# Optimization experiments

Hardware: AMD Instinct MI355X
Metric: run time of the kernel (lower is better)

Reference implementation:

```python
import jax, jax.numpy as jnp
import numpy as np

N, E, D, NHID, NOUT, G = 50000, 800000, 128, 512, 768, 512
EPS = 1e-5

def setup_inputs() -> dict:
    key = jax.random.key(0)
    ks = jax.random.split(key, 20)
    rn = lambda k, s: jax.random.normal(k, s, jnp.float32) * 0.05
    inp = {
        'x': jax.random.normal(ks[0], (N, D), jnp.float32),
        'edge_index': jax.random.randint(ks[1], (2, E), 0, N, jnp.int32),
        'batch': jnp.sort(jax.random.randint(ks[2], (N,), 0, G, jnp.int32)),
        # GCN convs 1..3 (weights stored [in, out])
        'W1': rn(ks[3], (D, D)), 'b1': jnp.zeros((D,), jnp.float32),
        'W2': rn(ks[4], (D, D)), 'b2': jnp.zeros((D,), jnp.float32),
        'W3': rn(ks[5], (D, D)), 'b3': jnp.zeros((D,), jnp.float32),
        # GAT attention layer (1 head)
        'Wa': rn(ks[6], (D, D)), 'ba': jnp.zeros((D,), jnp.float32),
        'a_src': rn(ks[7], (D,)), 'a_dst': rn(ks[8], (D,)),
        # BatchNorms: bn1, bn2, bn3, bn_attention stacked [4, D]
        'bn_gamma': jnp.ones((4, D), jnp.float32),
        'bn_beta': jnp.zeros((4, D), jnp.float32),
        # MLP head
        'Wm1': rn(ks[9], (D, NHID)), 'bm1': jnp.zeros((NHID,), jnp.float32),
        'Wm2': rn(ks[10], (NHID, NHID)), 'bm2': jnp.zeros((NHID,), jnp.float32),
        'Wm3': rn(ks[11], (NHID, NHID)), 'bm3': jnp.zeros((NHID,), jnp.float32),
        'Wm4': rn(ks[12], (NHID, NOUT)), 'bm4': jnp.zeros((NOUT,), jnp.float32),
    }
    return inp

def _bn(h, g, b):
    # BatchNorm1d over nodes, training-mode batch stats (biased variance)
    m = jnp.mean(h, axis=0)
    v = jnp.var(h, axis=0)
    return (h - m) * jax.lax.rsqrt(v + EPS) * g + b

def _gcn(x, W, b, src, dst, deg_isqrt):
    h = x @ W                               # [N, D]
    norm = deg_isqrt[src] * deg_isqrt[dst]  # [E+N]
    msg = h[src] * norm[:, None]            # gather + scale
    return jax.ops.segment_sum(msg, dst, num_segments=N) + b

def _gat(x, W, b, a_src, a_dst, src, dst):
    h = x @ W
    e = jax.nn.leaky_relu((h @ a_src)[src] + (h @ a_dst)[dst], 0.2)  # [E+N]
    m = jax.ops.segment_max(e, dst, num_segments=N)
    ex = jnp.exp(e - m[dst])
    den = jax.ops.segment_sum(ex, dst, num_segments=N)
    alpha = ex / den[dst]
    out = jax.ops.segment_sum(alpha[:, None] * h[src], dst, num_segments=N)
    return out + b

def reference(x, edge_index, batch, W1, b1, W2, b2, W3, b3, Wa, ba, a_src, a_dst,
              bn_gamma, bn_beta, Wm1, bm1, Wm2, bm2, Wm3, bm3, Wm4, bm4):
    # add self-loops (PyG GCNConv / GATConv default)
    loops = jnp.arange(N, dtype=edge_index.dtype)
    src = jnp.concatenate([edge_index[0], loops])
    dst = jnp.concatenate([edge_index[1], loops])
    deg = jax.ops.segment_sum(jnp.ones_like(dst, jnp.float32), dst, num_segments=N)
    deg_isqrt = jax.lax.rsqrt(deg)  # deg >= 1 thanks to self-loops

    relu = jax.nn.relu
    x = relu(_bn(_gcn(x, W1, b1, src, dst, deg_isqrt), bn_gamma[0], bn_beta[0])) + x
    x = relu(_bn(_gcn(x, W2, b2, src, dst, deg_isqrt), bn_gamma[1], bn_beta[1])) + x
    x = relu(_bn(_gcn(x, W3, b3, src, dst, deg_isqrt), bn_gamma[2], bn_beta[2])) + x
    x = relu(_bn(_gat(x, Wa, ba, a_src, a_dst, src, dst), bn_gamma[3], bn_beta[3])) + x

    # global mean pool over graphs
    counts = jax.ops.segment_sum(jnp.ones((N,), jnp.float32), batch, num_segments=G)
    pooled = jax.ops.segment_sum(x, batch, num_segments=G) / jnp.maximum(counts, 1.0)[:, None]

    h = relu(pooled @ Wm1 + bm1)
    h = relu(h @ Wm2 + bm2)
    h = relu(h @ Wm3 + bm3)
    return h @ Wm4 + bm4
```

## Files before the change

### kernel.cpp

```cpp
#include <hip/hip_runtime.h>
#include <stdint.h>

#define Nn   50000
#define Ee   800000
#define Dd   128
#define Gg   512
#define NHIDc 512
#define NOUTc 768
#define EPSf 1e-5f
#define CAP  64
#define PRNG 6250

#define OFF_CNT    0ul
#define OFF_ISQ    200192ul
#define OFF_ES     400384ul
#define OFF_ED     600576ul
#define OFF_STATS  800768ul
#define OFF_POOLED 801792ul
#define OFF_M1     1063936ul
#define OFF_M2     2112512ul
#define OFF_COL    3161088ul
#define OFF_H      15961088ul
#define OFF_AGG    28761088ul
#define OFF_XCUR   41561088ul

#define BF_LO(u) __uint_as_float((u) << 16)
#define BF_HI(u) __uint_as_float((u) & 0xffff0000u)

typedef __attribute__((ext_vector_type(8))) short bf16x8;
typedef __attribute__((ext_vector_type(4))) float f32x4;

__device__ inline uint32_t bfpack(float x, float y) {
    uint32_t ux = __float_as_uint(x), uy = __float_as_uint(y);
    ux += 0x7fff + ((ux >> 16) & 1);
    uy += 0x7fff + ((uy >> 16) & 1);
    return (ux >> 16) | (uy & 0xffff0000u);
}
__device__ inline short bf1(float x) {
    uint32_t u = __float_as_uint(x);
    u += 0x7fff + ((u >> 16) & 1);
    return (short)(u >> 16);
}
__device__ inline float wred16(float v) {
    v += __shfl_xor(v, 1); v += __shfl_xor(v, 2);
    v += __shfl_xor(v, 4); v += __shfl_xor(v, 8);
    return v;
}

__global__ void k_fill_init(int* cnt, int* colx) {
    int i = blockIdx.x * 256 + threadIdx.x;
    if (i < Nn) {
        cnt[i] = 1;
        colx[(size_t)i * CAP] = i;
    }
}

__global__ void k_bucket_fill(const int* __restrict__ ei, int* cnt, int* colx) {
    int grp = blockIdx.x & 7;
    int e = (blockIdx.x >> 3) * 256 + threadIdx.x;
    if (e >= Ee) return;
    int d = ei[Ee + e];
    if (d / PRNG != grp) return;
    int s = ei[e];
    int pos = atomicAdd(&cnt[d], 1);
    if (pos < CAP) colx[(size_t)d * CAP + pos] = s;
}

__global__ void k_isq(const int* __restrict__ cnt, float* __restrict__ isq) {
    int i = blockIdx.x * 256 + threadIdx.x;
    if (i < Nn) isq[i] = rsqrtf((float)cnt[i]);
}

#define WTP 136
__global__ __launch_bounds__(512) void k_gemm_fused(
        const float* __restrict__ X32, const uint32_t* __restrict__ XP,
        const uint32_t* __restrict__ AggP, const float* __restrict__ stats,
        const float* __restrict__ W, const float* __restrict__ isq,
        uint32_t* __restrict__ Hout, uint32_t* __restrict__ XoutP,
        const float* __restrict__ a_src, const float* __restrict__ a_dst,
        float* __restrict__ esO, float* __restrict__ edO) {
    __shared__ short WT[128 * WTP];
    __shared__ short XT[8][16 * WTP];
    __shared__ float isqL[128];

    int t = threadIdx.x;
    for (int i = t; i < 128 * 128; i += 512) {
        int k = i >> 7, c = i & 127;
        WT[c * WTP + k] = bf1(W[i]);
    }
    __syncthreads();

    int wave = t >> 6, lane = t & 63;
    int arow = lane & 15, kg = lane >> 4;
    float sc0 = 0.f, sh0 = 0.f, sc1 = 0.f, sh1 = 0.f;
    if (stats) {
        sc0 = stats[2 * lane];     sh0 = stats[128 + 2 * lane];
        sc1 = stats[2 * lane + 1]; sh1 = stats[129 + 2 * lane];
    }
    float asr[8], adr[8];
    if (esO) {
        #pragma unroll
        for (int jj = 0; jj < 8; ++jj) {
            asr[jj] = a_src[(lane & 15) * 8 + jj];
            adr[jj] = a_dst[(lane & 15) * 8 + jj];
        }
    }

    for (int tile = blockIdx.x * 128; tile < Nn; tile += gridDim.x * 128) {
        int rbase = tile + wave * 16;
        if (lane < 16) {
            int rg = rbase + lane;
            isqL[wave * 16 + lane] = (isq && rg < Nn) ? isq[rg] : 1.f;
        }
        for (int r = 0; r < 16; ++r) {
            int rg = rbase + r;
            float xn0 = 0.f, xn1 = 0.f;
            if (rg < Nn) {
                float px, py;
                if (X32) {
                    float2 xp = *reinterpret_cast<const float2*>(X32 + (size_t)rg * Dd + 2 * lane);
                    px = xp.x; py = xp.y;
                } else {
                    uint32_t ux = XP[(size_t)rg * 64 + lane];
                    px = BF_LO(ux); py = BF_HI(ux);
                }
                if (AggP) {
                    uint32_t ua = AggP[(size_t)rg * 64 + lane];
                    xn0 = fmaxf(BF_LO(ua) * sc0 + sh0, 0.f) + px;
                    xn1 = fmaxf(BF_HI(ua) * sc1 + sh1, 0.f) + py;
                    XoutP[(size_t)rg * 64 + lane] = bfpack(xn0, xn1);
                } else { xn0 = px; xn1 = py; }
            }
            *reinterpret_cast<uint32_t*>(&XT[wave][r * WTP + 2 * lane]) = bfpack(xn0, xn1);
        }
        bf16x8 afr[4];
        #pragma unroll
        for (int kt = 0; kt < 4; ++kt)
            afr[kt] = *reinterpret_cast<bf16x8*>(&XT[wave][arow * WTP + kt * 32 + kg * 8]);
        float sR[4];
        #pragma unroll
        for (int rr = 0; rr < 4; ++rr) sR[rr] = isqL[wave * 16 + kg * 4 + rr];

        #pragma unroll
        for (int ct = 0; ct < 8; ++ct) {
            int c = ct * 16 + arow;
            f32x4 acc = {0.f, 0.f, 0.f, 0.f};
            #pragma unroll
            for (int kt = 0; kt < 4; ++kt) {
                bf16x8 b = *reinterpret_cast<bf16x8*>(&WT[c * WTP + kt * 32 + kg * 8]);
                acc = __builtin_amdgcn_mfma_f32_16x16x32_bf16(afr[kt], b, acc, 0, 0, 0);
            }
            #pragma unroll
            for (int rr = 0; rr < 4; ++rr)
                XT[wave][(kg * 4 + rr) * WTP + c] = bf1(acc[rr] * sR[rr]);
        }
        #pragma unroll
        for (int p = 0; p < 4; ++p) {
            int rsl = p * 4 + kg;
            int rg = rbase + rsl;
            if (rg < Nn) {
                int chunk = lane & 15;
                bf16x8 vv = *reinterpret_cast<bf16x8*>(&XT[wave][rsl * WTP + chunk * 8]);
                *reinterpret_cast<bf16x8*>(reinterpret_cast<short*>(Hout) + (size_t)rg * 128 + chunk * 8) = vv;
                if (esO) {
                    float dsum = 0.f, ddum = 0.f;
                    #pragma unroll
                    for (int jj = 0; jj < 8; ++jj) {
                        float hv = __uint_as_float(((uint32_t)(unsigned short)vv[jj]) << 16);
                        dsum += hv * asr[jj];
                        ddum += hv * adr[jj];
                    }
                    dsum = wred16(dsum); ddum = wred16(ddum);
                    if ((lane & 15) == 0) { esO[rg] = dsum; edO[rg] = ddum; }
                }
            }
        }
    }
}

__global__ __launch_bounds__(256) void k_gcn_agg(const uint32_t* __restrict__ H,
                                                 const int* __restrict__ cnt,
                                                 const int* __restrict__ colx,
                                                 const float* __restrict__ isq,
                                                 uint32_t* __restrict__ aggP) {
    int nid = blockIdx.x * 4 + (threadIdx.x >> 6);
    if (nid >= Nn) return;
    int lane = threadIdx.x & 63;
    int half = lane >> 5, fl = lane & 31;
    int deg = cnt[nid]; if (deg > CAP) deg = CAP;
    size_t cb = (size_t)nid * CAP;
    const uint2* H2 = reinterpret_cast<const uint2*>(H);

    int m = (deg - half + 1) >> 1;
    float f0a = 0.f, f1a = 0.f, f2a = 0.f, f3a = 0.f;
    float f0b = 0.f, f1b = 0.f, f2b = 0.f, f3b = 0.f;
    float f0c = 0.f, f1c = 0.f, f2c = 0.f, f3c = 0.f;
    float f0d = 0.f, f1d = 0.f, f2d = 0.f, f3d = 0.f;
    int k = 0;
    for (; k + 3 < m; k += 4) {
        int s0 = colx[cb + half + 2 * k];
        int s1 = colx[cb + half + 2 * k + 2];
        int s2 = colx[cb + half + 2 * k + 4];
        int s3 = colx[cb + half + 2 * k + 6];
        uint2 u0 = H2[(size_t)s0 * 32 + fl];
        uint2 u1 = H2[(size_t)s1 * 32 + fl];
        uint2 u2 = H2[(size_t)s2 * 32 + fl];
        uint2 u3 = H2[(size_t)s3 * 32 + fl];
        f0a += BF_LO(u0.x); f1a += BF_HI(u0.x); f2a += BF_LO(u0.y); f3a += BF_HI(u0.y);
        f0b += BF_LO(u1.x); f1b += BF_HI(u1.x); f2b += BF_LO(u1.y); f3b += BF_HI(u1.y);
        f0c += BF_LO(u2.x); f1c += BF_HI(u2.x); f2c += BF_LO(u2.y); f3c += BF_HI(u2.y);
        f0d += BF_LO(u3.x); f1d += BF_HI(u3.x); f2d += BF_LO(u3.y); f3d += BF_HI(u3.y);
    }
    for (; k < m; ++k) {
        int s0 = colx[cb + half + 2 * k];
        uint2 u0 = H2[(size_t)s0 * 32 + fl];
        f0a += BF_LO(u0.x); f1a += BF_HI(u0.x); f2a += BF_LO(u0.y); f3a += BF_HI(u0.y);
    }
    float f0 = (f0a + f0b) + (f0c + f0d);
    float f1 = (f1a + f1b) + (f1c + f1d);
    float f2 = (f2a + f2b) + (f2c + f2d);
    float f3 = (f3a + f3b) + (f3c + f3d);
    f0 += __shfl_xor(f0, 32); f1 += __shfl_xor(f1, 32);
    f2 += __shfl_xor(f2, 32); f3 += __shfl_xor(f3, 32);
    if (half == 0) {
        float wd = isq[nid];
        uint2 o;
        o.x = bfpack(f0 * wd, f1 * wd);
        o.y = bfpack(f2 * wd, f3 * wd);
        reinterpret_cast<uint2*>(aggP)[(size_t)nid * 32 + fl] = o;
    }
}

__global__ __launch_bounds__(256) void k_gat_agg(const uint32_t* __restrict__ H,
                                                 const int* __restrict__ cnt,
                                                 const int* __restrict__ colx,
                                                 const float* __restrict__ es,
                                                 const float* __restrict__ ed,
                                                 uint32_t* __restrict__ aggP) {
    int nid = blockIdx.x * 4 + (threadIdx.x >> 6);
    if (nid >= Nn) return;
    int lane = threadIdx.x & 63;
    int half = lane >> 5, fl = lane & 31;
    int deg = cnt[nid]; if (deg > CAP) deg = CAP;
    size_t cb = (size_t)nid * CAP;
    const uint2* H2 = reinterpret_cast<const uint2*>(H);
    float edd = ed[nid];

    int m = (deg - half + 1) >> 1;
    float f0a = 0.f, f1a = 0.f, f2a = 0.f, f3a = 0.f, dena = 0.f;
    float f0b = 0.f, f1b = 0.f, f2b = 0.f, f3b = 0.f, denb = 0.f;
    float f0c = 0.f, f1c = 0.f, f2c = 0.f, f3c = 0.f, denc = 0.f;
    float f0d = 0.f, f1d = 0.f, f2d = 0.f, f3d = 0.f, dend = 0.f;
    int k = 0;
    for (; k + 3 < m; k += 4) {
        int s0 = colx[cb + half + 2 * k];
        int s1 = colx[cb + half + 2 * k + 2];
        int s2 = colx[cb + half + 2 * k + 4];
        int s3 = colx[cb + half + 2 * k + 6];
        float e0 = es[s0] + edd, e1 = es[s1] + edd;
        float e2 = es[s2] + edd, e3 = es[s3] + edd;
        e0 = (e0 < 0.f) ? 0.2f * e0 : e0;
        e1 = (e1 < 0.f) ? 0.2f * e1 : e1;
        e2 = (e2 < 0.f) ? 0.2f * e2 : e2;
        e3 = (e3 < 0.f) ? 0.2f * e3 : e3;
        float w0 = __expf(e0), w1 = __expf(e1), w2 = __expf(e2), w3 = __expf(e3);
        uint2 u0 = H2[(size_t)s0 * 32 + fl];
        uint2 u1 = H2[(size_t)s1 * 32 + fl];
        uint2 u2 = H2[(size_t)s2 * 32 + fl];
        uint2 u3 = H2[(size_t)s3 * 32 + fl];
        f0a += w0 * BF_LO(u0.x); f1a += w0 * BF_HI(u0.x);
        f2a += w0 * BF_LO(u0.y); f3a += w0 * BF_HI(u0.y); dena += w0;
        f0b += w1 * BF_LO(u1.x); f1b += w1 * BF_HI(u1.x);
        f2b += w1 * BF_LO(u1.y); f3b += w1 * BF_HI(u1.y); denb += w1;
        f0c += w2 * BF_LO(u2.x); f1c += w2 * BF_HI(u2.x);
        f2c += w2 * BF_LO(u2.y); f3c += w2 * BF_HI(u2.y); denc += w2;
        f0d += w3 * BF_LO(u3.x); f1d += w3 * BF_HI(u3.x);
        f2d += w3 * BF_LO(u3.y); f3d += w3 * BF_HI(u3.y); dend += w3;
    }
    for (; k < m; ++k) {
        int s0 = colx[cb + half + 2 * k];
        float e0 = es[s0] + edd;
        e0 = (e0 < 0.f) ? 0.2f * e0 : e0;
        float w0 = __expf(e0);
        uint2 u0 = H2[(size_t)s0 * 32 + fl];
        f0a += w0 * BF_LO(u0.x); f1a += w0 * BF_HI(u0.x);
        f2a += w0 * BF_LO(u0.y); f3a += w0 * BF_HI(u0.y); dena += w0;
    }
    float f0 = (f0a + f0b) + (f0c + f0d);
    float f1 = (f1a + f1b) + (f1c + f1d);
    float f2 = (f2a + f2b) + (f2c + f2d);
    float f3 = (f3a + f3b) + (f3c + f3d);
    float den = (dena + denb) + (denc + dend);
    f0 += __shfl_xor(f0, 32); f1 += __shfl_xor(f1, 32);
    f2 += __shfl_xor(f2, 32); f3 += __shfl_xor(f3, 32);
    den += __shfl_xor(den, 32);
    if (half == 0) {
        float inv = 1.f / den;
        uint2 o;
        o.x = bfpack(f0 * inv, f1 * inv);
        o.y = bfpack(f2 * inv, f3 * inv);
        reinterpret_cast<uint2*>(aggP)[(size_t)nid * 32 + fl] = o;
    }
}

__global__ __launch_bounds__(256) void k_bn_stats(const uint32_t* __restrict__ AP,
                                                  float* __restrict__ part) {
    int t = threadIdx.x;
    int w = t & 63, rg = t >> 6;
    float sl = 0.f, s2l = 0.f, sh = 0.f, s2h = 0.f;
    for (int r = blockIdx.x * 4 + rg; r < Nn; r += gridDim.x * 4) {
        uint32_t u = AP[(size_t)r * 64 + w];
        float a = BF_LO(u), b = BF_HI(u);
        sl += a; s2l += a * a; sh += b; s2h += b * b;
    }
    __shared__ float rA[256], rB[256], rC[256], rD[256];
    rA[t] = sl; rB[t] = s2l; rC[t] = sh; rD[t] = s2h;
    __syncthreads();
    if (t < 64) {
        float S  = rA[t] + rA[t + 64] + rA[t + 128] + rA[t + 192];
        float S2 = rB[t] + rB[t + 64] + rB[t + 128] + rB[t + 192];
        float T  = rC[t] + rC[t + 64] + rC[t + 128] + rC[t + 192];
        float T2 = rD[t] + rD[t + 64] + rD[t + 128] + rD[t + 192];
        part[blockIdx.x * 256 + 2 * t]           = S;
        part[blockIdx.x * 256 + 2 * t + 1]       = T;
        part[blockIdx.x * 256 + 128 + 2 * t]     = S2;
        part[blockIdx.x * 256 + 128 + 2 * t + 1] = T2;
    }
}

__global__ void k_bn_final(const float* __restrict__ part, float* stats,
                           const float* __restrict__ gamma, const float* __restrict__ beta) {
    int f = threadIdx.x;
    if (f >= 128) return;
    float s = 0.f, s2 = 0.f;
    for (int b = 0; b < 256; ++b) {
        s += part[b * 256 + f];
        s2 += part[b * 256 + 128 + f];
    }
    const float invN = 1.f / (float)Nn;
    float mean = s * invN;
    float var = s2 * invN - mean * mean;
    float scv = rsqrtf(var + EPSf) * gamma[f];
    stats[f] = scv;
    stats[128 + f] = beta[f] - mean * scv;
}

__global__ __launch_bounds__(256) void k_pool(const uint32_t* __restrict__ AP,
                                              const float* __restrict__ stats,
                                              const uint32_t* __restrict__ XcP,
                                              const int* __restrict__ batch,
                                              float* __restrict__ pooled) {
    int g = blockIdx.x;
    int lo = 0, hi = Nn;
    while (lo < hi) { int mid = (lo + hi) >> 1; if (batch[mid] < g) lo = mid + 1; else hi = mid; }
    int start = lo;
    lo = start; hi = Nn;
    while (lo < hi) { int mid = (lo + hi) >> 1; if (batch[mid] < g + 1) lo = mid + 1; else hi = mid; }
    int end = lo;

    int f = threadIdx.x & 127, rg = threadIdx.x >> 7;
    float sc = stats[f], sh = stats[128 + f];
    float s = 0.f;
    for (int r = start + rg; r < end; r += 2) {
        uint32_t u = AP[(size_t)r * 64 + (f >> 1)];
        uint32_t ux = XcP[(size_t)r * 64 + (f >> 1)];
        float a  = (f & 1) ? BF_HI(u)  : BF_LO(u);
        float xv = (f & 1) ? BF_HI(ux) : BF_LO(ux);
        s += fmaxf(a * sc + sh, 0.f) + xv;
    }
    __shared__ float red[256];
    red[threadIdx.x] = s; __syncthreads();
    if (threadIdx.x < 128) {
        float tot = red[threadIdx.x] + red[threadIdx.x + 128];
        float cntg = (float)(end - start);
        pooled[g * Dd + threadIdx.x] = (cntg > 0.f) ? tot / cntg : 0.f;
    }
}

__global__ __launch_bounds__(256) void k_mlp32(const float* __restrict__ A,
                                               const float* __restrict__ B,
                                               const float* __restrict__ bias,
                                               float* __restrict__ C,
                                               int M, int K, int Nc, int do_relu) {
    __shared__ float Ast[64][36];
    __shared__ float Bs[64][68];

    int nbx = Nc >> 6;
    int by = blockIdx.x / nbx, bx = blockIdx.x - by * nbx;
    int r0 = by * 32, c0 = bx * 64;
    int t = threadIdx.x;
    int tc = t & 31, tr = t >> 5;

    float2 acc0 = {0, 0}, acc1 = {0, 0}, acc2 = {0, 0}, acc3 = {0, 0};

    int sar = t >> 3, sak = (t & 7) * 8;
    int sbk = t >> 2, sbc = (t & 3) * 16;

    for (int kc = 0; kc < K; kc += 64) {
        {
            const float* ap = A + (size_t)(r0 + sar) * K + kc + sak;
            float4 v0 = *reinterpret_cast<const float4*>(ap);
            float4 v1 = *reinterpret_cast<const float4*>(ap + 4);
            Ast[sak + 0][sar] = v0.x; Ast[sak + 1][sar] = v0.y;
            Ast[sak + 2][sar] = v0.z; Ast[sak + 3][sar] = v0.w;
            Ast[sak + 4][sar] = v1.x; Ast[sak + 5][sar] = v1.y;
            Ast[sak + 6][sar] = v1.z; Ast[sak + 7][sar] = v1.w;
        }
        {
            const float* bp = B + (size_t)(kc + sbk) * Nc + c0 + sbc;
            float4 w0 = *reinterpret_cast<const float4*>(bp);
            float4 w1 = *reinterpret_cast<const float4*>(bp + 4);
            float4 w2 = *reinterpret_cast<const float4*>(bp + 8);
            float4 w3 = *reinterpret_cast<const float4*>(bp + 12);
            *reinterpret_cast<float4*>(&Bs[sbk][sbc]) = w0;
            *reinterpret_cast<float4*>(&Bs[sbk][sbc + 4]) = w1;
            *reinterpret_cast<float4*>(&Bs[sbk][sbc + 8]) = w2;
            *reinterpret_cast<float4*>(&Bs[sbk][sbc + 12]) = w3;
        }
        __syncthreads();
        #pragma unroll 8
        for (int k = 0; k < 64; ++k) {
            float4 a = *reinterpret_cast<float4*>(&Ast[k][tr * 4]);
            float2 b = *reinterpret_cast<float2*>(&Bs[k][tc * 2]);
            acc0.x += a.x * b.x; acc0.y += a.x * b.y;
            acc1.x += a.y * b.x; acc1.y += a.y * b.y;
            acc2.x += a.z * b.x; acc2.y += a.z * b.y;
            acc3.x += a.w * b.x; acc3.y += a.w * b.y;
        }
        __syncthreads();
    }

    float b0 = bias[c0 + tc * 2], b1 = bias[c0 + tc * 2 + 1];
    float2 r[4] = {{acc0.x + b0, acc0.y + b1}, {acc1.x + b0, acc1.y + b1},
                   {acc2.x + b0, acc2.y + b1}, {acc3.x + b0, acc3.y + b1}};
    if (do_relu) {
        #pragma unroll
        for (int i = 0; i < 4; ++i) {
            r[i].x = fmaxf(r[i].x, 0.f); r[i].y = fmaxf(r[i].y, 0.f);
        }
    }
    #pragma unroll
    for (int i = 0; i < 4; ++i)
        *reinterpret_cast<float2*>(C + (size_t)(r0 + tr * 4 + i) * Nc + c0 + tc * 2) = r[i];
}

extern "C" void kernel_launch(void* const* d_in, const int* in_sizes, int n_in,
                              void* d_out, int out_size, void* d_ws, size_t ws_size,
                              hipStream_t stream) {
    const float* x       = (const float*)d_in[0];
    const int*   ei      = (const int*)d_in[1];
    const int*   batch   = (const int*)d_in[2];
    const float* W1      = (const float*)d_in[3];
    const float* W2      = (const float*)d_in[5];
    const float* W3      = (const float*)d_in[7];
    const float* Wa      = (const float*)d_in[9];
    const float* a_src   = (const float*)d_in[11];
    const float* a_dst   = (const float*)d_in[12];
    const float* bn_g    = (const float*)d_in[13];
    const float* bn_b    = (const float*)d_in[14];
    const float* Wm1     = (const float*)d_in[15];
    const float* bm1     = (const float*)d_in[16];
    const float* Wm2     = (const float*)d_in[17];
    const float* bm2     = (const float*)d_in[18];
    const float* Wm3     = (const float*)d_in[19];
    const float* bm3     = (const float*)d_in[20];
    const float* Wm4     = (const float*)d_in[21];
    const float* bm4     = (const float*)d_in[22];

    char* ws = (char*)d_ws;
    int*      cnt    = (int*)(ws + OFF_CNT);
    float*    isq    = (float*)(ws + OFF_ISQ);
    float*    es     = (float*)(ws + OFF_ES);
    float*    ed     = (float*)(ws + OFF_ED);
    float*    stats  = (float*)(ws + OFF_STATS);
    float*    pooled = (float*)(ws + OFF_POOLED);
    float*    m1     = (float*)(ws + OFF_M1);
    float*    m2     = (float*)(ws + OFF_M2);
    int*      colx   = (int*)(ws + OFF_COL);
    uint32_t* h      = (uint32_t*)(ws + OFF_H);
    uint32_t* aggP   = (uint32_t*)(ws + OFF_AGG);
    uint32_t* xcurP  = (uint32_t*)(ws + OFF_XCUR);

    const int nb196 = 196;
    const int nbE8  = ((Ee + 255) / 256) * 8;
    const int nbNode = (Nn + 3) / 4;
    const int nbGemm = (Nn + 127) / 128;

    k_fill_init<<<nb196, 256, 0, stream>>>(cnt, colx);
    k_bucket_fill<<<nbE8, 256, 0, stream>>>(ei, cnt, colx);
    k_isq<<<nb196, 256, 0, stream>>>(cnt, isq);

    k_gemm_fused<<<nbGemm, 512, 0, stream>>>(x, nullptr, nullptr, nullptr, W1, isq, h, nullptr,
                                             nullptr, nullptr, nullptr, nullptr);
    k_gcn_agg<<<nbNode, 256, 0, stream>>>(h, cnt, colx, isq, aggP);
    k_bn_stats<<<256, 256, 0, stream>>>(aggP, m1);
    k_bn_final<<<1, 128, 0, stream>>>(m1, stats, bn_g + 0 * Dd, bn_b + 0 * Dd);

    k_gemm_fused<<<nbGemm, 512, 0, stream>>>(x, nullptr, aggP, stats, W2, isq, h, xcurP,
                                             nullptr, nullptr, nullptr, nullptr);
    k_gcn_agg<<<nbNode, 256, 0, stream>>>(h, cnt, colx, isq, aggP);
    k_bn_stats<<<256, 256, 0, stream>>>(aggP, m1);
    k_bn_final<<<1, 128, 0, stream>>>(m1, stats, bn_g + 1 * Dd, bn_b + 1 * Dd);

    k_gemm_fused<<<nbGemm, 512, 0, stream>>>(nullptr, xcurP, aggP, stats, W3, isq, h, xcurP,
                                             nullptr, nullptr, nullptr, nullptr);
    k_gcn_agg<<<nbNode, 256, 0, stream>>>(h, cnt, colx, isq, aggP);
    k_bn_stats<<<256, 256, 0, stream>>>(aggP, m1);
    k_bn_final<<<1, 128, 0, stream>>>(m1, stats, bn_g + 2 * Dd, bn_b + 2 * Dd);

    k_gemm_fused<<<nbGemm, 512, 0, stream>>>(nullptr, xcurP, aggP, stats, Wa, nullptr, h, xcurP,
                                             a_src, a_dst, es, ed);
    k_gat_agg<<<nbNode, 256, 0, stream>>>(h, cnt, colx, es, ed, aggP);
    k_bn_stats<<<256, 256, 0, stream>>>(aggP, m1);
    k_bn_final<<<1, 128, 0, stream>>>(m1, stats, bn_g + 3 * Dd, bn_b + 3 * Dd);

    k_pool<<<Gg, 256, 0, stream>>>(aggP, stats, xcurP, batch, pooled);

    k_mlp32<<<(Gg / 32) * (NHIDc / 64), 256, 0, stream>>>(pooled, Wm1, bm1, m1, Gg, Dd, NHIDc, 1);
    k_mlp32<<<(Gg / 32) * (NHIDc / 64), 256, 0, stream>>>(m1, Wm2, bm2, m2, Gg, NHIDc, NHIDc, 1);
    k_mlp32<<<(Gg / 32) * (NHIDc / 64), 256, 0, stream>>>(m2, Wm3, bm3, m1, Gg, NHIDc, NHIDc, 1);
    k_mlp32<<<(Gg / 32) * (NOUTc / 64), 256, 0, stream>>>(m1, Wm4, bm4, (float*)d_out, Gg, NHIDc, NOUTc, 0);
}
```

Before: 449.6 us.

## Fuse BatchNorm statistics into aggregation kernels and drop isq kernel

The GCN and GAT aggregation kernels become grid-stride loops over 2048 blocks. Each accumulates per-feature sum and sum-of-squares of its fp32 outputs and writes per-block partials, which removes the separate k_bn_stats pass that re-read the aggregated bf16 tensor. The k_isq kernel is dropped, and rsqrt of the degree is computed inline in the GEMM and aggregation kernels. k_bn_final is widened to 1024 threads to reduce the 2048 partials. Stats are now taken from pre-rounding fp32 values, which differs slightly from the old bf16-based stats, and the partials buffer reuses m1.

```diff
diff --git a/kernel.cpp b/kernel.cpp
--- a/kernel.cpp
+++ b/kernel.cpp
@@ -10,19 +10,19 @@
 #define EPSf 1e-5f
 #define CAP  64
 #define PRNG 6250
+#define NBAGG 2048
 
 #define OFF_CNT    0ul
-#define OFF_ISQ    200192ul
-#define OFF_ES     400384ul
-#define OFF_ED     600576ul
-#define OFF_STATS  800768ul
-#define OFF_POOLED 801792ul
-#define OFF_M1     1063936ul
-#define OFF_M2     2112512ul
-#define OFF_COL    3161088ul
-#define OFF_H      15961088ul
-#define OFF_AGG    28761088ul
-#define OFF_XCUR   41561088ul
+#define OFF_ES     200192ul
+#define OFF_ED     400384ul
+#define OFF_STATS  600576ul
+#define OFF_POOLED 601600ul
+#define OFF_M1     863744ul
+#define OFF_M2     1912320ul
+#define OFF_COL    2960896ul
+#define OFF_H      15760896ul
+#define OFF_AGG    28560896ul
+#define OFF_XCUR   41360896ul
 
 #define BF_LO(u) __uint_as_float((u) << 16)
 #define BF_HI(u) __uint_as_float((u) & 0xffff0000u)
@@ -66,16 +66,11 @@
     if (pos < CAP) colx[(size_t)d * CAP + pos] = s;
 }
 
-__global__ void k_isq(const int* __restrict__ cnt, float* __restrict__ isq) {
-    int i = blockIdx.x * 256 + threadIdx.x;
-    if (i < Nn) isq[i] = rsqrtf((float)cnt[i]);
-}
-
 #define WTP 136
 __global__ __launch_bounds__(512) void k_gemm_fused(
         const float* __restrict__ X32, const uint32_t* __restrict__ XP,
         const uint32_t* __restrict__ AggP, const float* __restrict__ stats,
-        const float* __restrict__ W, const float* __restrict__ isq,
+        const float* __restrict__ W, const int* __restrict__ cntP,
         uint32_t* __restrict__ Hout, uint32_t* __restrict__ XoutP,
         const float* __restrict__ a_src, const float* __restrict__ a_dst,
         float* __restrict__ esO, float* __restrict__ edO) {
@@ -110,7 +105,7 @@
         int rbase = tile + wave * 16;
         if (lane < 16) {
             int rg = rbase + lane;
-            isqL[wave * 16 + lane] = (isq && rg < Nn) ? isq[rg] : 1.f;
+            isqL[wave * 16 + lane] = (cntP && rg < Nn) ? rsqrtf((float)cntP[rg]) : 1.f;
         }
         for (int r = 0; r < 16; ++r) {
             int rg = rbase + r;
@@ -181,53 +176,75 @@
 __global__ __launch_bounds__(256) void k_gcn_agg(const uint32_t* __restrict__ H,
                                                  const int* __restrict__ cnt,
                                                  const int* __restrict__ colx,
-                                                 const float* __restrict__ isq,
-                                                 uint32_t* __restrict__ aggP) {
-    int nid = blockIdx.x * 4 + (threadIdx.x >> 6);
-    if (nid >= Nn) return;
-    int lane = threadIdx.x & 63;
+                                                 uint32_t* __restrict__ aggP,
+                                                 float* __restrict__ part) {
+    int wave = threadIdx.x >> 6, lane = threadIdx.x & 63;
     int half = lane >> 5, fl = lane & 31;
-    int deg = cnt[nid]; if (deg > CAP) deg = CAP;
-    size_t cb = (size_t)nid * CAP;
     const uint2* H2 = reinterpret_cast<const uint2*>(H);
-
-    int m = (deg - half + 1) >> 1;
-    float f0a = 0.f, f1a = 0.f, f2a = 0.f, f3a = 0.f;
-    float f0b = 0.f, f1b = 0.f, f2b = 0.f, f3b = 0.f;
-    float f0c = 0.f, f1c = 0.f, f2c = 0.f, f3c = 0.f;
-    float f0d = 0.f, f1d = 0.f, f2d = 0.f, f3d = 0.f;
-    int k = 0;
-    for (; k + 3 < m; k += 4) {
-        int s0 = colx[cb + half + 2 * k];
-        int s1 = colx[cb + half + 2 * k + 2];
-        int s2 = colx[cb + half + 2 * k + 4];
-        int s3 = colx[cb + half + 2 * k + 6];
-        uint2 u0 = H2[(size_t)s0 * 32 + fl];
-        uint2 u1 = H2[(size_t)s1 * 32 + fl];
-        uint2 u2 = H2[(size_t)s2 * 32 + fl];
-        uint2 u3 = H2[(size_t)s3 * 32 + fl];
-        f0a += BF_LO(u0.x); f1a += BF_HI(u0.x); f2a += BF_LO(u0.y); f3a += BF_HI(u0.y);
-        f0b += BF_LO(u1.x); f1b += BF_HI(u1.x); f2b += BF_LO(u1.y); f3b += BF_HI(u1.y);
-        f0c += BF_LO(u2.x); f1c += BF_HI(u2.x); f2c += BF_LO(u2.y); f3c += BF_HI(u2.y);
-        f0d += BF_LO(u3.x); f1d += BF_HI(u3.x); f2d += BF_LO(u3.y); f3d += BF_HI(u3.y);
-    }
-    for (; k < m; ++k) {
-        int s0 = colx[cb + half + 2 * k];
-        uint2 u0 = H2[(size_t)s0 * 32 + fl];
-        f0a += BF_LO(u0.x); f1a += BF_HI(u0.x); f2a += BF_LO(u0.y); f3a += BF_HI(u0.y);
-    }
-    float f0 = (f0a + f0b) + (f0c + f0d);
-    float f1 = (f1a + f1b) + (f1c + f1d);
-    float f2 = (f2a + f2b) + (f2c + f2d);
-    float f3 = (f3a + f3b) + (f3c + f3d);
-    f0 += __shfl_xor(f0, 32); f1 += __shfl_xor(f1, 32);
-    f2 += __shfl_xor(f2, 32); f3 += __shfl_xor(f3, 32);
+    float sAcc0 = 0.f, sAcc1 = 0.f, sAcc2 = 0.f, sAcc3 = 0.f;
+    float qAcc0 = 0.f, qAcc1 = 0.f, qAcc2 = 0.f, qAcc3 = 0.f;
+
+    for (int nid = blockIdx.x * 4 + wave; nid < Nn; nid += gridDim.x * 4) {
+        int degF = cnt[nid];
+        int deg = degF > CAP ? CAP : degF;
+        size_t cb = (size_t)nid * CAP;
+        int m = (deg - half + 1) >> 1;
+        float f0a = 0.f, f1a = 0.f, f2a = 0.f, f3a = 0.f;
+        float f0b = 0.f, f1b = 0.f, f2b = 0.f, f3b = 0.f;
+        float f0c = 0.f, f1c = 0.f, f2c = 0.f, f3c = 0.f;
+        float f0d = 0.f, f1d = 0.f, f2d = 0.f, f3d = 0.f;
+        int k = 0;
+        for (; k + 3 < m; k += 4) {
+            int s0 = colx[cb + half + 2 * k];
+            int s1 = colx[cb + half + 2 * k + 2];
+            int s2 = colx[cb + half + 2 * k + 4];
+            int s3 = colx[cb + half + 2 * k + 6];
+            uint2 u0 = H2[(size_t)s0 * 32 + fl];
+            uint2 u1 = H2[(size_t)s1 * 32 + fl];
+            uint2 u2 = H2[(size_t)s2 * 32 + fl];
+            uint2 u3 = H2[(size_t)s3 * 32 + fl];
+            f0a += BF_LO(u0.x); f1a += BF_HI(u0.x); f2a += BF_LO(u0.y); f3a += BF_HI(u0.y);
+            f0b += BF_LO(u1.x); f1b += BF_HI(u1.x); f2b += BF_LO(u1.y); f3b += BF_HI(u1.y);
+            f0c += BF_LO(u2.x); f1c += BF_HI(u2.x); f2c += BF_LO(u2.y); f3c += BF_HI(u2.y);
+            f0d += BF_LO(u3.x); f1d += BF_HI(u3.x); f2d += BF_LO(u3.y); f3d += BF_HI(u3.y);
+        }
+        for (; k < m; ++k) {
+            int s0 = colx[cb + half + 2 * k];
+            uint2 u0 = H2[(size_t)s0 * 32 + fl];
+            f0a += BF_LO(u0.x); f1a += BF_HI(u0.x); f2a += BF_LO(u0.y); f3a += BF_HI(u0.y);
+        }
+        float f0 = (f0a + f0b) + (f0c + f0d);
+        float f1 = (f1a + f1b) + (f1c + f1d);
+        float f2 = (f2a + f2b) + (f2c + f2d);
+        float f3 = (f3a + f3b) + (f3c + f3d);
+        f0 += __shfl_xor(f0, 32); f1 += __shfl_xor(f1, 32);
+        f2 += __shfl_xor(f2, 32); f3 += __shfl_xor(f3, 32);
+        if (half == 0) {
+            float wd = rsqrtf((float)degF);
+            float o0 = f0 * wd, o1 = f1 * wd, o2 = f2 * wd, o3 = f3 * wd;
+            uint2 o;
+            o.x = bfpack(o0, o1);
+            o.y = bfpack(o2, o3);
+            reinterpret_cast<uint2*>(aggP)[(size_t)nid * 32 + fl] = o;
+            sAcc0 += o0; qAcc0 += o0 * o0;
+            sAcc1 += o1; qAcc1 += o1 * o1;
+            sAcc2 += o2; qAcc2 += o2 * o2;
+            sAcc3 += o3; qAcc3 += o3 * o3;
+        }
+    }
+    __shared__ float SS[4][128];
+    __shared__ float QQ[4][128];
     if (half == 0) {
-        float wd = isq[nid];
-        uint2 o;
-        o.x = bfpack(f0 * wd, f1 * wd);
-        o.y = bfpack(f2 * wd, f3 * wd);
-        reinterpret_cast<uint2*>(aggP)[(size_t)nid * 32 + fl] = o;
+        SS[wave][4 * fl + 0] = sAcc0; QQ[wave][4 * fl + 0] = qAcc0;
+        SS[wave][4 * fl + 1] = sAcc1; QQ[wave][4 * fl + 1] = qAcc1;
+        SS[wave][4 * fl + 2] = sAcc2; QQ[wave][4 * fl + 2] = qAcc2;
+        SS[wave][4 * fl + 3] = sAcc3; QQ[wave][4 * fl + 3] = qAcc3;
+    }
+    __syncthreads();
+    int t = threadIdx.x;
+    if (t < 128) {
+        part[blockIdx.x * 256 + t]       = (SS[0][t] + SS[1][t]) + (SS[2][t] + SS[3][t]);
+        part[blockIdx.x * 256 + 128 + t] = (QQ[0][t] + QQ[1][t]) + (QQ[2][t] + QQ[3][t]);
     }
 }
 
@@ -236,113 +253,121 @@
                                                  const int* __restrict__ colx,
                                                  const float* __restrict__ es,
                                                  const float* __restrict__ ed,
-                                                 uint32_t* __restrict__ aggP) {
-    int nid = blockIdx.x * 4 + (threadIdx.x >> 6);
-    if (nid >= Nn) return;
-    int lane = threadIdx.x & 63;
+                                                 uint32_t* __restrict__ aggP,
+                                                 float* __restrict__ part) {
+    int wave = threadIdx.x >> 6, lane = threadIdx.x & 63;
     int half = lane >> 5, fl = lane & 31;
-    int deg = cnt[nid]; if (deg > CAP) deg = CAP;
-    size_t cb = (size_t)nid * CAP;
     const uint2* H2 = reinterpret_cast<const uint2*>(H);
-    float edd = ed[nid];
-
-    int m = (deg - half + 1) >> 1;
-    float f0a = 0.f, f1a = 0.f, f2a = 0.f, f3a = 0.f, dena = 0.f;
-    float f0b = 0.f, f1b = 0.f, f2b = 0.f, f3b = 0.f, denb = 0.f;
-    float f0c = 0.f, f1c = 0.f, f2c = 0.f, f3c = 0.f, denc = 0.f;
-    float f0d = 0.f, f1d = 0.f, f2d = 0.f, f3d = 0.f, dend = 0.f;
-    int k = 0;
-    for (; k + 3 < m; k += 4) {
-        int s0 = colx[cb + half + 2 * k];
-        int s1 = colx[cb + half + 2 * k + 2];
-        int s2 = colx[cb + half + 2 * k + 4];
-        int s3 = colx[cb + half + 2 * k + 6];
-        float e0 = es[s0] + edd, e1 = es[s1] + edd;
-        float e2 = es[s2] + edd, e3 = es[s3] + edd;
-        e0 = (e0 < 0.f) ? 0.2f * e0 : e0;
-        e1 = (e1 < 0.f) ? 0.2f * e1 : e1;
-        e2 = (e2 < 0.f) ? 0.2f * e2 : e2;
-        e3 = (e3 < 0.f) ? 0.2f * e3 : e3;
-        float w0 = __expf(e0), w1 = __expf(e1), w2 = __expf(e2), w3 = __expf(e3);
-        uint2 u0 = H2[(size_t)s0 * 32 + fl];
-        uint2 u1 = H2[(size_t)s1 * 32 + fl];
-        uint2 u2 = H2[(size_t)s2 * 32 + fl];
-        uint2 u3 = H2[(size_t)s3 * 32 + fl];
-        f0a += w0 * BF_LO(u0.x); f1a += w0 * BF_HI(u0.x);
-        f2a += w0 * BF_LO(u0.y); f3a += w0 * BF_HI(u0.y); dena += w0;
-        f0b += w1 * BF_LO(u1.x); f1b += w1 * BF_HI(u1.x);
-        f2b += w1 * BF_LO(u1.y); f3b += w1 * BF_HI(u1.y); denb += w1;
-        f0c += w2 * BF_LO(u2.x); f1c += w2 * BF_HI(u2.x);
-        f2c += w2 * BF_LO(u2.y); f3c += w2 * BF_HI(u2.y); denc += w2;
-        f0d += w3 * BF_LO(u3.x); f1d += w3 * BF_HI(u3.x);
-        f2d += w3 * BF_LO(u3.y); f3d += w3 * BF_HI(u3.y); dend += w3;
-    }
-    for (; k < m; ++k) {
-        int s0 = colx[cb + half + 2 * k];
-        float e0 = es[s0] + edd;
-        e0 = (e0 < 0.f) ? 0.2f * e0 : e0;
-        float w0 = __expf(e0);
-        uint2 u0 = H2[(size_t)s0 * 32 + fl];
-        f0a += w0 * BF_LO(u0.x); f1a += w0 * BF_HI(u0.x);
-        f2a += w0 * BF_LO(u0.y); f3a += w0 * BF_HI(u0.y); dena += w0;
-    }
-    float f0 = (f0a + f0b) + (f0c + f0d);
-    float f1 = (f1a + f1b) + (f1c + f1d);
-    float f2 = (f2a + f2b) + (f2c + f2d);
-    float f3 = (f3a + f3b) + (f3c + f3d);
-    float den = (dena + denb) + (denc + dend);
-    f0 += __shfl_xor(f0, 32); f1 += __shfl_xor(f1, 32);
-    f2 += __shfl_xor(f2, 32); f3 += __shfl_xor(f3, 32);
-    den += __shfl_xor(den, 32);
+    float sAcc0 = 0.f, sAcc1 = 0.f, sAcc2 = 0.f, sAcc3 = 0.f;
+    float qAcc0 = 0.f, qAcc1 = 0.f, qAcc2 = 0.f, qAcc3 = 0.f;
+
+    for (int nid = blockIdx.x * 4 + wave; nid < Nn; nid += gridDim.x * 4) {
+        int degF = cnt[nid];
+        int deg = degF > CAP ? CAP : degF;
+        size_t cb = (size_t)nid * CAP;
+        float edd = ed[nid];
+        int m = (deg - half + 1) >> 1;
+        float f0a = 0.f, f1a = 0.f, f2a = 0.f, f3a = 0.f, dena = 0.f;
+        float f0b = 0.f, f1b = 0.f, f2b = 0.f, f3b = 0.f, denb = 0.f;
+        float f0c = 0.f, f1c = 0.f, f2c = 0.f, f3c = 0.f, denc = 0.f;
+        float f0d = 0.f, f1d = 0.f, f2d = 0.f, f3d = 0.f, dend = 0.f;
+        int k = 0;
+        for (; k + 3 < m; k += 4) {
+            int s0 = colx[cb + half + 2 * k];
+            int s1 = colx[cb + half + 2 * k + 2];
+            int s2 = colx[cb + half + 2 * k + 4];
+            int s3 = colx[cb + half + 2 * k + 6];
+            float e0 = es[s0] + edd, e1 = es[s1] + edd;
+            float e2 = es[s2] + edd, e3 = es[s3] + edd;
+            e0 = (e0 < 0.f) ? 0.2f * e0 : e0;
+            e1 = (e1 < 0.f) ? 0.2f * e1 : e1;
+            e2 = (e2 < 0.f) ? 0.2f * e2 : e2;
+            e3 = (e3 < 0.f) ? 0.2f * e3 : e3;
+            float w0 = __expf(e0), w1 = __expf(e1), w2 = __expf(e2), w3 = __expf(e3);
+            uint2 u0 = H2[(size_t)s0 * 32 + fl];
+            uint2 u1 = H2[(size_t)s1 * 32 + fl];
+            uint2 u2 = H2[(size_t)s2 * 32 + fl];
+            uint2 u3 = H2[(size_t)s3 * 32 + fl];
+            f0a += w0 * BF_LO(u0.x); f1a += w0 * BF_HI(u0.x);
+            f2a += w0 * BF_LO(u0.y); f3a += w0 * BF_HI(u0.y); dena += w0;
+            f0b += w1 * BF_LO(u1.x); f1b += w1 * BF_HI(u1.x);
+            f2b += w1 * BF_LO(u1.y); f3b += w1 * BF_HI(u1.y); denb += w1;
+            f0c += w2 * BF_LO(u2.x); f1c += w2 * BF_HI(u2.x);
+            f2c += w2 * BF_LO(u2.y); f3c += w2 * BF_HI(u2.y); denc += w2;
+            f0d += w3 * BF_LO(u3.x); f1d += w3 * BF_HI(u3.x);
+            f2d += w3 * BF_LO(u3.y); f3d += w3 * BF_HI(u3.y); dend += w3;
+        }
+        for (; k < m; ++k) {
+            int s0 = colx[cb + half + 2 * k];
+            float e0 = es[s0] + edd;
+            e0 = (e0 < 0.f) ? 0.2f * e0 : e0;
+            float w0 = __expf(e0);
+            uint2 u0 = H2[(size_t)s0 * 32 + fl];
+            f0a += w0 * BF_LO(u0.x); f1a += w0 * BF_HI(u0.x);
+            f2a += w0 * BF_LO(u0.y); f3a += w0 * BF_HI(u0.y); dena += w0;
+        }
+        float f0 = (f0a + f0b) + (f0c + f0d);
+        float f1 = (f1a + f1b) + (f1c + f1d);
+        float f2 = (f2a + f2b) + (f2c + f2d);
+        float f3 = (f3a + f3b) + (f3c + f3d);
+        float den = (dena + denb) + (denc + dend);
+        f0 += __shfl_xor(f0, 32); f1 += __shfl_xor(f1, 32);
+        f2 += __shfl_xor(f2, 32); f3 += __shfl_xor(f3, 32);
+        den += __shfl_xor(den, 32);
+        if (half == 0) {
+            float inv = 1.f / den;
+            float o0 = f0 * inv, o1 = f1 * inv, o2 = f2 * inv, o3 = f3 * inv;
+            uint2 o;
+            o.x = bfpack(o0, o1);
+            o.y = bfpack(o2, o3);
+            reinterpret_cast<uint2*>(aggP)[(size_t)nid * 32 + fl] = o;
+            sAcc0 += o0; qAcc0 += o0 * o0;
+            sAcc1 += o1; qAcc1 += o1 * o1;
+            sAcc2 += o2; qAcc2 += o2 * o2;
+            sAcc3 += o3; qAcc3 += o3 * o3;
+        }
+    }
+    __shared__ float SS[4][128];
+    __shared__ float QQ[4][128];
     if (half == 0) {
-        float inv = 1.f / den;
-        uint2 o;
-        o.x = bfpack(f0 * inv, f1 * inv);
-        o.y = bfpack(f2 * inv, f3 * inv);
-        reinterpret_cast<uint2*>(aggP)[(size_t)nid * 32 + fl] = o;
-    }
-}
-
-__global__ __launch_bounds__(256) void k_bn_stats(const uint32_t* __restrict__ AP,
-                                                  float* __restrict__ part) {
+        SS[wave][4 * fl + 0] = sAcc0; QQ[wave][4 * fl + 0] = qAcc0;
+        SS[wave][4 * fl + 1] = sAcc1; QQ[wave][4 * fl + 1] = qAcc1;
+        SS[wave][4 * fl + 2] = sAcc2; QQ[wave][4 * fl + 2] = qAcc2;
+        SS[wave][4 * fl + 3] = sAcc3; QQ[wave][4 * fl + 3] = qAcc3;
+    }
+    __syncthreads();
     int t = threadIdx.x;
-    int w = t & 63, rg = t >> 6;
-    float sl = 0.f, s2l = 0.f, sh = 0.f, s2h = 0.f;
-    for (int r = blockIdx.x * 4 + rg; r < Nn; r += gridDim.x * 4) {
-        uint32_t u = AP[(size_t)r * 64 + w];
-        float a = BF_LO(u), b = BF_HI(u);
-        sl += a; s2l += a * a; sh += b; s2h += b * b;
-    }
-    __shared__ float rA[256], rB[256], rC[256], rD[256];
-    rA[t] = sl; rB[t] = s2l; rC[t] = sh; rD[t] = s2h;
+    if (t < 128) {
+        part[blockIdx.x * 256 + t]       = (SS[0][t] + SS[1][t]) + (SS[2][t] + SS[3][t]);
+        part[blockIdx.x * 256 + 128 + t] = (QQ[0][t] + QQ[1][t]) + (QQ[2][t] + QQ[3][t]);
+    }
+}
+
+__global__ __launch_bounds__(1024) void k_bn_final(const float* __restrict__ part, float* stats,
+                                                   const float* __restrict__ gamma,
+                                                   const float* __restrict__ beta) {
+    __shared__ float LS[8][128];
+    __shared__ float LQ[8][128];
+    int t = threadIdx.x;
+    int grp = t >> 7, f = t & 127;
+    float s = 0.f, q = 0.f;
+    for (int b = grp; b < NBAGG; b += 8) {
+        s += part[b * 256 + f];
+        q += part[b * 256 + 128 + f];
+    }
+    LS[grp][f] = s; LQ[grp][f] = q;
     __syncthreads();
-    if (t < 64) {
-        float S  = rA[t] + rA[t + 64] + rA[t + 128] + rA[t + 192];
-        float S2 = rB[t] + rB[t + 64] + rB[t + 128] + rB[t + 192];
-        float T  = rC[t] + rC[t + 64] + rC[t + 128] + rC[t + 192];
-        float T2 = rD[t] + rD[t + 64] + rD[t + 128] + rD[t + 192];
-        part[blockIdx.x * 256 + 2 * t]           = S;
-        part[blockIdx.x * 256 + 2 * t + 1]       = T;
-        part[blockIdx.x * 256 + 128 + 2 * t]     = S2;
-        part[blockIdx.x * 256 + 128 + 2 * t + 1] = T2;
-    }
-}
-
-__global__ void k_bn_final(const float* __restrict__ part, float* stats,
-                           const float* __restrict__ gamma, const float* __restrict__ beta) {
-    int f = threadIdx.x;
-    if (f >= 128) return;
-    float s = 0.f, s2 = 0.f;
-    for (int b = 0; b < 256; ++b) {
-        s += part[b * 256 + f];
-        s2 += part[b * 256 + 128 + f];
-    }
-    const float invN = 1.f / (float)Nn;
-    float mean = s * invN;
-    float var = s2 * invN - mean * mean;
-    float scv = rsqrtf(var + EPSf) * gamma[f];
-    stats[f] = scv;
-    stats[128 + f] = beta[f] - mean * scv;
+    if (t < 128) {
+        float S = 0.f, Q = 0.f;
+        #pragma unroll
+        for (int g2 = 0; g2 < 8; ++g2) { S += LS[g2][t]; Q += LQ[g2][t]; }
+        const float invN = 1.f / (float)Nn;
+        float mean = S * invN;
+        float var = Q * invN - mean * mean;
+        float scv = rsqrtf(var + EPSf) * gamma[t];
+        stats[t] = scv;
+        stats[128 + t] = beta[t] - mean * scv;
+    }
 }
 
 __global__ __launch_bounds__(256) void k_pool(const uint32_t* __restrict__ AP,
@@ -469,7 +494,6 @@
 
     char* ws = (char*)d_ws;
     int*      cnt    = (int*)(ws + OFF_CNT);
-    float*    isq    = (float*)(ws + OFF_ISQ);
     float*    es     = (float*)(ws + OFF_ES);
     float*    ed     = (float*)(ws + OFF_ED);
     float*    stats  = (float*)(ws + OFF_STATS);
@@ -480,39 +504,34 @@
     uint32_t* h      = (uint32_t*)(ws + OFF_H);
     uint32_t* aggP   = (uint32_t*)(ws + OFF_AGG);
     uint32_t* xcurP  = (uint32_t*)(ws + OFF_XCUR);
+    float*    part   = m1;
 
     const int nb196 = 196;
     const int nbE8  = ((Ee + 255) / 256) * 8;
-    const int nbNode = (Nn + 3) / 4;
     const int nbGemm = (Nn + 127) / 128;
 
     k_fill_init<<<nb196, 256, 0, stream>>>(cnt, colx);
     k_bucket_fill<<<nbE8, 256, 0, stream>>>(ei, cnt, colx);
-    k_isq<<<nb196, 256, 0, stream>>>(cnt, isq);
-
-    k_gemm_fused<<<nbGemm, 512, 0, stream>>>(x, nullptr, nullptr, nullptr, W1, isq, h, nullptr,
+
+    k_gemm_fused<<<nbGemm, 512, 0, stream>>>(x, nullptr, nullptr, nullptr, W1, cnt, h, nullptr,
                                              nullptr, nullptr, nullptr, nullptr);
-    k_gcn_agg<<<nbNode, 256, 0, stream>>>(h, cnt, colx, isq, aggP);
-    k_bn_stats<<<256, 256, 0, stream>>>(aggP, m1);
-    k_bn_final<<<1, 128, 0, stream>>>(m1, stats, bn_g + 0 * Dd, bn_b + 0 * Dd);
-
-    k_gemm_fused<<<nbGemm, 512, 0, stream>>>(x, nullptr, aggP, stats, W2, isq, h, xcurP,
+    k_gcn_agg<<<NBAGG, 256, 0, stream>>>(h, cnt, colx, aggP, part);
+    k_bn_final<<<1, 1024, 0, stream>>>(part, stats, bn_g + 0 * Dd, bn_b + 0 * Dd);
+
+    k_gemm_fused<<<nbGemm, 512, 0, stream>>>(x, nullptr, aggP, stats, W2, cnt, h, xcurP,
                                              nullptr, nullptr, nullptr, nullptr);
-    k_gcn_agg<<<nbNode, 256, 0, stream>>>(h, cnt, colx, isq, aggP);
-    k_bn_stats<<<256, 256, 0, stream>>>(aggP, m1);
-    k_bn_final<<<1, 128, 0, stream>>>(m1, stats, bn_g + 1 * Dd, bn_b + 1 * Dd);
-
-    k_gemm_fused<<<nbGemm, 512, 0, stream>>>(nullptr, xcurP, aggP, stats, W3, isq, h, xcurP,
+    k_gcn_agg<<<NBAGG, 256, 0, stream>>>(h, cnt, colx, aggP, part);
+    k_bn_final<<<1, 1024, 0, stream>>>(part, stats, bn_g + 1 * Dd, bn_b + 1 * Dd);
+
+    k_gemm_fused<<<nbGemm, 512, 0, stream>>>(nullptr, xcurP, aggP, stats, W3, cnt, h, xcurP,
                                              nullptr, nullptr, nullptr, nullptr);
-    k_gcn_agg<<<nbNode, 256, 0, stream>>>(h, cnt, colx, isq, aggP);
-    k_bn_stats<<<256, 256, 0, stream>>>(aggP, m1);
-    k_bn_final<<<1, 128, 0, stream>>>(m1, stats, bn_g + 2 * Dd, bn_b + 2 * Dd);
+    k_gcn_agg<<<NBAGG, 256, 0, stream>>>(h, cnt, colx, aggP, part);
+    k_bn_final<<<1, 1024, 0, stream>>>(part, stats, bn_g + 2 * Dd, bn_b + 2 * Dd);
 
     k_gemm_fused<<<nbGemm, 512, 0, stream>>>(nullptr, xcurP, aggP, stats, Wa, nullptr, h, xcurP,
                                              a_src, a_dst, es, ed);
-    k_gat_agg<<<nbNode, 256, 0, stream>>>(h, cnt, colx, es, ed, aggP);
-    k_bn_stats<<<256, 256, 0, stream>>>(aggP, m1);
-    k_bn_final<<<1, 128, 0, stream>>>(m1, stats, bn_g + 3 * Dd, bn_b + 3 * Dd);
+    k_gat_agg<<<NBAGG, 256, 0, stream>>>(h, cnt, colx, es, ed, aggP, part);
+    k_bn_final<<<1, 1024, 0, stream>>>(part, stats, bn_g + 3 * Dd, bn_b + 3 * Dd);
 
     k_pool<<<Gg, 256, 0, stream>>>(aggP, stats, xcurP, batch, pooled);
 
```

New measurement: 705.5 us. 1.57x slower.
